# Kernel optimization log

Hardware: AMD Instinct MI355X
Metric: run time of the kernel (lower is better)

Reference implementation:

```python
import jax, jax.numpy as jnp
import numpy as np

QUERY_DIM = 1024
KEY_DIM = 768
NUM_HEADS = 16
HEAD_DIM = QUERY_DIM // NUM_HEADS


def _linear_params(key, in_dim, out_dim):
    kw, kb = jax.random.split(key)
    bound = 1.0 / np.sqrt(in_dim)
    W = jax.random.uniform(kw, (out_dim, in_dim), minval=-bound, maxval=bound, dtype=jnp.float32)
    b = jax.random.uniform(kb, (out_dim,), minval=-bound, maxval=bound, dtype=jnp.float32)
    return W, b


def setup_inputs() -> dict:
    key = jax.random.key(0)
    ks = jax.random.split(key, 7)
    B, Nq, Nk = 4, 1024, 2048
    query = jax.random.normal(ks[0], (B, Nq, QUERY_DIM), dtype=jnp.float32)
    k_in = jax.random.normal(ks[1], (B, Nk, KEY_DIM), dtype=jnp.float32)
    v_in = jax.random.normal(ks[2], (B, Nk, KEY_DIM), dtype=jnp.float32)
    Wq, bq = _linear_params(ks[3], QUERY_DIM, QUERY_DIM)
    Wk, bk = _linear_params(ks[4], KEY_DIM, QUERY_DIM)
    Wv, bv = _linear_params(ks[5], KEY_DIM, QUERY_DIM)
    Wo, bo = _linear_params(ks[6], QUERY_DIM, QUERY_DIM)
    return {
        "query": query, "key": k_in, "value": v_in,
        "Wq": Wq, "bq": bq, "Wk": Wk, "bk": bk,
        "Wv": Wv, "bv": bv, "Wo": Wo, "bo": bo,
    }


def reference(query, key, value, Wq, bq, Wk, bk, Wv, bv, Wo, bo):
    B, Nq, _ = query.shape
    Nk = key.shape[1]
    H, D = NUM_HEADS, HEAD_DIM
    scale = 1.0 / np.sqrt(D)
    # Projections (torch Linear: x @ W.T + b), then split heads -> (B, H, N, D)
    Q = (query @ Wq.T + bq).reshape(B, Nq, H, D).transpose(0, 2, 1, 3)
    K = (key @ Wk.T + bk).reshape(B, Nk, H, D).transpose(0, 2, 1, 3)
    V = (value @ Wv.T + bv).reshape(B, Nk, H, D).transpose(0, 2, 1, 3)
    # Explicit score matrix (B, H, Nq, Nk), softmax over keys
    attn = jnp.einsum('bhqd,bhkd->bhqk', Q, K) * scale
    attn = jax.nn.softmax(attn, axis=-1)
    out = jnp.einsum('bhqk,bhkd->bhqd', attn, V)
    out = out.transpose(0, 2, 1, 3).reshape(B, Nq, H * D)
    return out @ Wo.T + bo
```

## Files before the change

kernel.cpp:

```cpp
#include <hip/hip_runtime.h>
#include <stdint.h>


typedef __attribute__((ext_vector_type(4))) float f32x4;
typedef __attribute__((ext_vector_type(8))) _Float16 half8;
typedef __attribute__((ext_vector_type(4))) _Float16 half4;
typedef __attribute__((ext_vector_type(4))) short short4v;
typedef __attribute__((ext_vector_type(8))) short short8;
typedef unsigned short u16;

__device__ __forceinline__ u16 f2h(float f){
  _Float16 h = (_Float16)f;
  return __builtin_bit_cast(unsigned short, h);
}

__device__ __forceinline__ void gload16(const void* g, void* lds){
  __builtin_amdgcn_global_load_lds((const __attribute__((address_space(1))) void*)g,
                                   (__attribute__((address_space(3))) void*)lds, 16, 0, 0);
}

struct Seg { const float* s; u16* d; int n4; };
struct Cvt7 { Seg seg[7]; };

__global__ __launch_bounds__(256) void cvt_f32_f16(Cvt7 a){
  Seg sg = a.seg[blockIdx.y];
  const long stride = (long)gridDim.x * 256;
  for (long i = (long)blockIdx.x*256 + threadIdx.x; i < sg.n4; i += stride){
    f32x4 v = *(const f32x4*)(sg.s + i*4);
    short4v h;
    h[0] = (short)f2h(v[0]); h[1] = (short)f2h(v[1]);
    h[2] = (short)f2h(v[2]); h[3] = (short)f2h(v[3]);
    *(short4v*)(sg.d + i*4) = h;
  }
}

template<int R, int THREADS>
__device__ __forceinline__ void stage_tile(const char* gbase, long gstride, char* lds, int tid){
  const int w = tid >> 6, lane = tid & 63;
  #pragma unroll
  for (int it = 0; it < R*8/THREADS; ++it){
    int c  = it*THREADS + w*64 + lane;
    int r  = c >> 3;
    int bs = (c & 7) << 4;
    int sb = bs ^ ((r & 7) << 4);
    gload16(gbase + (long)r*gstride + sb, lds + (it*THREADS + w*64)*16);
  }
}

__device__ __forceinline__ void gemm64_mainloop(const u16* A, const u16* Bt, int K,
                                                int row0, int col0, int tid,
                                                char* Alds, char* Blds, f32x4 acc[2][4]){
  const int lane = tid & 63, w = tid >> 6;
  const int g = lane >> 4, lm = lane & 15;
  const int wr = (w >> 1) * 32, wc = (w & 1) * 64;
  const char* Ag = (const char*)A  + ((long)row0 * K) * 2;
  const char* Bg = (const char*)Bt + ((long)col0 * K) * 2;
  for (int k0 = 0; k0 < K; k0 += 64){
    stage_tile<64, 256>(Ag + k0*2, (long)K*2, Alds, tid);
    stage_tile<128, 256>(Bg + k0*2, (long)K*2, Blds, tid);
    __syncthreads();
    #pragma unroll
    for (int kk = 0; kk < 2; ++kk){
      half8 af[2], bfr[4];
      #pragma unroll
      for (int mi = 0; mi < 2; ++mi){
        int r = wr + mi*16 + lm;
        af[mi] = *(const half8*)(Alds + r*128 + ((kk*64 + g*16) ^ ((r & 7) << 4)));
      }
      #pragma unroll
      for (int ni = 0; ni < 4; ++ni){
        int r = wc + ni*16 + lm;
        bfr[ni] = *(const half8*)(Blds + r*128 + ((kk*64 + g*16) ^ ((r & 7) << 4)));
      }
      #pragma unroll
      for (int mi = 0; mi < 2; ++mi)
        #pragma unroll
        for (int ni = 0; ni < 4; ++ni)
          acc[mi][ni] = __builtin_amdgcn_mfma_f32_16x16x32_f16(af[mi], bfr[ni], acc[mi][ni], 0, 0, 0);
    }
    __syncthreads();
  }
}

__global__ __launch_bounds__(256, 4)
void qkv_proj(const u16* __restrict__ qH, const u16* __restrict__ kH, const u16* __restrict__ vH,
              const u16* __restrict__ WqH, const u16* __restrict__ WkH, const u16* __restrict__ WvH,
              const float* __restrict__ bq, const float* __restrict__ bk, const float* __restrict__ bv,
              u16* __restrict__ Qw, u16* __restrict__ Kw, u16* __restrict__ Vtw)
{
  __shared__ __align__(128) char Alds[8192];
  __shared__ __align__(128) char Blds[16384];
  const int tid = threadIdx.x, lane = tid & 63, w = tid >> 6;
  const int g = lane >> 4, lm = lane & 15;

  int bid = blockIdx.x;
  const u16 *A, *Bt; const float* bias; u16* out16;
  int K, logS, local; float scale = 1.0f;
  int which;
  if (bid < 512)       { which = 0; local = bid;        A = qH; Bt = WqH; bias = bq; out16 = Qw;  K = 1024; logS = 10; scale = 0.125f; }
  else if (bid < 1536) { which = 1; local = bid - 512;  A = kH; Bt = WkH; bias = bk; out16 = Kw;  K = 768;  logS = 11; }
  else                 { which = 2; local = bid - 1536; A = vH; Bt = WvH; bias = bv; out16 = Vtw; K = 768;  logS = 11; }
  const int rb = local >> 3, cb = local & 7;
  const int row0 = rb * 64, col0 = cb * 128;

  f32x4 acc[2][4];
  #pragma unroll
  for (int i = 0; i < 2; ++i)
    #pragma unroll
    for (int j = 0; j < 4; ++j) acc[i][j] = {0.f, 0.f, 0.f, 0.f};

  gemm64_mainloop(A, Bt, K, row0, col0, tid, Alds, Blds, acc);

  const int wr = (w >> 1) * 32, wc = (w & 1) * 64;
  if (which != 2){
    #pragma unroll
    for (int mi = 0; mi < 2; ++mi)
      #pragma unroll
      for (int ni = 0; ni < 4; ++ni){
        int n = col0 + wc + ni*16 + lm;
        float bvv = bias[n];
        int h_ = n >> 6, d_ = n & 63;
        #pragma unroll
        for (int r = 0; r < 4; ++r){
          int m = row0 + wr + mi*16 + g*4 + r;
          int b_ = m >> logS, s_ = m & ((1 << logS) - 1);
          long dst = (((long)(b_*16 + h_) << logS) + s_) * 64 + d_;
          out16[dst] = f2h((acc[mi][ni][r] + bvv) * scale);
        }
      }
  } else {
    #pragma unroll
    for (int mi = 0; mi < 2; ++mi)
      #pragma unroll
      for (int ni = 0; ni < 4; ++ni){
        int np = wc + ni*16 + lm;
        float bvv = bias[col0 + np];
        short4v h4;
        #pragma unroll
        for (int r = 0; r < 4; ++r) h4[r] = (short)f2h(acc[mi][ni][r] + bvv);
        int mb = (wr + mi*16 + g*4) * 2;
        *(short4v*)(Blds + np*128 + (mb ^ ((np & 7) << 4))) = h4;
      }
    __syncthreads();
    const int b_ = row0 >> 11;
    #pragma unroll
    for (int pass = 0; pass < 4; ++pass){
      int idx = pass*256 + tid, row = idx >> 3, c = idx & 7;
      short8 v = *(const short8*)(Blds + row*128 + ((c*16) ^ ((row & 7) << 4)));
      int ng = col0 + row, h_ = ng >> 6, d_ = ng & 63;
      long dst = ((long)(b_*16 + h_)*64 + d_)*2048 + (row0 & 2047) + c*8;
      *(short8*)(out16 + dst) = v;
    }
  }
}

__global__ __launch_bounds__(512, 4)
void attn_fused(const u16* __restrict__ Qw, const u16* __restrict__ Kw,
                const u16* __restrict__ Vtw, u16* __restrict__ AO)
{
  __shared__ __align__(128) char Klds[8192];
  __shared__ __align__(128) char Vlds[8192];
  const int tid = threadIdx.x, lane = tid & 63, w = tid >> 6;
  const int g = lane >> 4, lm = lane & 15;
  const int p = blockIdx.x;
  const int slot = p >> 3;
  const int bh = (p & 7) + ((slot & 7) << 3);
  const int qt = slot >> 3;
  const long qbase = (long)bh * 1024 * 64;
  const long kbase = (long)bh * 2048 * 64;
  const long vbase = (long)bh * 64 * 2048;

  const int q0 = qt*128 + w*16;
  half8 aQ[2];
  #pragma unroll
  for (int kk = 0; kk < 2; ++kk)
    aQ[kk] = *(const half8*)((const char*)Qw + (qbase + (long)(q0 + lm)*64 + kk*32 + g*8)*2);

  float mrun = -3e38f, lrun = 0.f;
  f32x4 O[4];
  #pragma unroll
  for (int di = 0; di < 4; ++di) O[di] = {0.f, 0.f, 0.f, 0.f};

  for (int kt = 0; kt < 2048; kt += 64){
    stage_tile<64, 512>((const char*)Kw  + (kbase + (long)kt*64)*2, 128,  Klds, tid);
    stage_tile<64, 512>((const char*)Vtw + (vbase + kt)*2,          4096, Vlds, tid);
    __syncthreads();

    half8 kf[4][2];
    #pragma unroll
    for (int t = 0; t < 4; ++t)
      #pragma unroll
      for (int kk = 0; kk < 2; ++kk){
        int r = t*16 + lm;
        kf[t][kk] = *(const half8*)(Klds + r*128 + ((kk*64 + g*16) ^ ((r & 7) << 4)));
      }

    f32x4 sc[4];
    #pragma unroll
    for (int t = 0; t < 4; ++t){
      f32x4 z = {0.f, 0.f, 0.f, 0.f};
      z = __builtin_amdgcn_mfma_f32_16x16x32_f16(kf[t][0], aQ[0], z, 0, 0, 0);
      z = __builtin_amdgcn_mfma_f32_16x16x32_f16(kf[t][1], aQ[1], z, 0, 0, 0);
      sc[t] = z;
    }
    float pm = sc[0][0];
    #pragma unroll
    for (int t = 0; t < 4; ++t)
      #pragma unroll
      for (int r = 0; r < 4; ++r) pm = fmaxf(pm, sc[t][r]);
    pm = fmaxf(pm, __shfl_xor(pm, 16));
    pm = fmaxf(pm, __shfl_xor(pm, 32));
    float mnew = fmaxf(mrun, pm);
    float fac  = __expf(mrun - mnew);
    float ls = 0.f;
    #pragma unroll
    for (int t = 0; t < 4; ++t)
      #pragma unroll
      for (int r = 0; r < 4; ++r){ float pv = __expf(sc[t][r] - mnew); sc[t][r] = pv; ls += pv; }
    ls += __shfl_xor(ls, 16);
    ls += __shfl_xor(ls, 32);
    lrun = lrun*fac + ls;
    mrun = mnew;
    float frow[4];
    #pragma unroll
    for (int r = 0; r < 4; ++r) frow[r] = __shfl(fac, (lane & 48) | (g*4 + r));
    #pragma unroll
    for (int di = 0; di < 4; ++di){
      O[di][0] *= frow[0]; O[di][1] *= frow[1];
      O[di][2] *= frow[2]; O[di][3] *= frow[3];
    }
    half8 pa[2];
    #pragma unroll
    for (int kh = 0; kh < 2; ++kh)
      #pragma unroll
      for (int i = 0; i < 8; ++i){
        int t = kh*2 + (i >> 2), r = i & 3;
        pa[kh][i] = (_Float16)sc[t][r];
      }
    #pragma unroll
    for (int di = 0; di < 4; ++di){
      int d = di*16 + lm;
      int swz = (d & 7) << 4;
      #pragma unroll
      for (int kh = 0; kh < 2; ++kh){
        half4 lo = *(const half4*)(Vlds + d*128 + ((kh*64 + g*8)      ^ swz));
        half4 hi = *(const half4*)(Vlds + d*128 + ((kh*64 + g*8 + 32) ^ swz));
        half8 vf = { lo[0], lo[1], lo[2], lo[3], hi[0], hi[1], hi[2], hi[3] };
        O[di] = __builtin_amdgcn_mfma_f32_16x16x32_f16(pa[kh], vf, O[di], 0, 0, 0);
      }
    }
    __syncthreads();
  }

  const int b = bh >> 4, h = bh & 15;
  float inv = 1.f / lrun;
  float irow[4];
  #pragma unroll
  for (int r = 0; r < 4; ++r) irow[r] = __shfl(inv, (lane & 48) | (g*4 + r));
  #pragma unroll
  for (int di = 0; di < 4; ++di)
    #pragma unroll
    for (int r = 0; r < 4; ++r){
      long q = q0 + g*4 + r;
      AO[((long)b*1024 + q)*1024 + h*64 + di*16 + lm] = f2h(O[di][r] * irow[r]);
    }
}

__global__ __launch_bounds__(256, 4)
void gemm_o(const u16* __restrict__ A, const u16* __restrict__ Bt,
            const float* __restrict__ bias, float* __restrict__ outF)
{
  __shared__ __align__(128) char Alds[8192];
  __shared__ __align__(128) char Blds[16384];
  const int tid = threadIdx.x, lane = tid & 63, w = tid >> 6;
  const int g = lane >> 4, lm = lane & 15;
  const int rb = blockIdx.x >> 3, cb = blockIdx.x & 7;
  const int row0 = rb * 64, col0 = cb * 128;

  f32x4 acc[2][4];
  #pragma unroll
  for (int i = 0; i < 2; ++i)
    #pragma unroll
    for (int j = 0; j < 4; ++j) acc[i][j] = {0.f, 0.f, 0.f, 0.f};

  gemm64_mainloop(A, Bt, 1024, row0, col0, tid, Alds, Blds, acc);

  const int wr = (w >> 1) * 32, wc = (w & 1) * 64;
  #pragma unroll
  for (int mi = 0; mi < 2; ++mi)
    #pragma unroll
    for (int ni = 0; ni < 4; ++ni){
      int n = col0 + wc + ni*16 + lm;
      float bvv = bias[n];
      #pragma unroll
      for (int r = 0; r < 4; ++r){
        int m = row0 + wr + mi*16 + g*4 + r;
        outF[(long)m * 1024 + n] = acc[mi][ni][r] + bvv;
      }
    }
}

extern "C" void kernel_launch(void* const* d_in, const int* in_sizes, int n_in,
                              void* d_out, int out_size, void* d_ws, size_t ws_size,
                              hipStream_t stream)
{
  const float* query = (const float*)d_in[0];
  const float* key   = (const float*)d_in[1];
  const float* value = (const float*)d_in[2];
  const float* Wq = (const float*)d_in[3];
  const float* bq = (const float*)d_in[4];
  const float* Wk = (const float*)d_in[5];
  const float* bk = (const float*)d_in[6];
  const float* Wv = (const float*)d_in[7];
  const float* bv = (const float*)d_in[8];
  const float* Wo = (const float*)d_in[9];
  const float* bo = (const float*)d_in[10];
  float* out = (float*)d_out;

  char* p = (char*)d_ws;
  auto alloc = [&](long bytes){ char* r = p; p += bytes; return r; };
  u16* qH  = (u16*)alloc( 8l<<20);
  u16* kH  = (u16*)alloc(12l<<20);
  u16* vH  = (u16*)alloc(12l<<20);
  u16* WqH = (u16*)alloc( 2l<<20);
  u16* WkH = (u16*)alloc( 2l<<20);
  u16* WvH = (u16*)alloc( 2l<<20);
  u16* WoH = (u16*)alloc( 2l<<20);
  u16* Qw  = (u16*)alloc( 8l<<20);
  u16* Kw  = (u16*)alloc(16l<<20);
  u16* Vtw = (u16*)alloc(16l<<20);
  u16* AO  = (u16*)alloc( 8l<<20);

  Cvt7 ca;
  ca.seg[0] = { query, qH,  4096*1024/4 };
  ca.seg[1] = { key,   kH,  8192*768/4  };
  ca.seg[2] = { value, vH,  8192*768/4  };
  ca.seg[3] = { Wq,    WqH, 1024*1024/4 };
  ca.seg[4] = { Wk,    WkH, 1024*768/4  };
  ca.seg[5] = { Wv,    WvH, 1024*768/4  };
  ca.seg[6] = { Wo,    WoH, 1024*1024/4 };
  cvt_f32_f16<<<dim3(512, 7), 256, 0, stream>>>(ca);

  qkv_proj<<<dim3(2560), dim3(256), 0, stream>>>(qH, kH, vH, WqH, WkH, WvH,
                                                 bq, bk, bv, Qw, Kw, Vtw);
  attn_fused<<<dim3(512), dim3(512), 0, stream>>>(Qw, Kw, Vtw, AO);
  gemm_o<<<dim3(512), dim3(256), 0, stream>>>(AO, WoH, bo, out);
}
```

Measured before the change: 267.6 us.

## Double-buffer LDS tiles, remap blocks for XCDs, add lazy softmax rescale

Both GEMM mainloops and the attention loop now use double-buffered LDS. The next K tile is issued with global_load_lds before the current tile is computed, and partial vmcnt waits with raw barriers replace the __syncthreads pairs. Block IDs in the QKV and output GEMMs are remapped so neighbouring tiles land on the same XCD. Attention skips the running-max rescale unless the new max exceeds the old by more than 8, and packs P to half with cvt_pkrtz. The doubled LDS lowers the GEMM occupancy hint from 4 to 3 blocks, and the lazy rescale allows somewhat larger intermediate values.

```diff
diff --git a/kernel.cpp b/kernel.cpp
--- a/kernel.cpp
+++ b/kernel.cpp
@@ -5,6 +5,7 @@
 typedef __attribute__((ext_vector_type(4))) float f32x4;
 typedef __attribute__((ext_vector_type(8))) _Float16 half8;
 typedef __attribute__((ext_vector_type(4))) _Float16 half4;
+typedef __attribute__((ext_vector_type(2))) _Float16 half2v;
 typedef __attribute__((ext_vector_type(4))) short short4v;
 typedef __attribute__((ext_vector_type(8))) short short8;
 typedef unsigned short u16;
@@ -47,30 +48,42 @@
   }
 }
 
-__device__ __forceinline__ void gemm64_mainloop(const u16* A, const u16* Bt, int K,
-                                                int row0, int col0, int tid,
-                                                char* Alds, char* Blds, f32x4 acc[2][4]){
+__device__ __forceinline__ void gemm64_pipe(const u16* A, const u16* Bt, int K,
+                                            int row0, int col0, int tid,
+                                            char* lds, f32x4 acc[2][4]){
   const int lane = tid & 63, w = tid >> 6;
   const int g = lane >> 4, lm = lane & 15;
   const int wr = (w >> 1) * 32, wc = (w & 1) * 64;
   const char* Ag = (const char*)A  + ((long)row0 * K) * 2;
   const char* Bg = (const char*)Bt + ((long)col0 * K) * 2;
+
+  stage_tile<64, 256>(Ag, (long)K*2, lds, tid);
+  stage_tile<128, 256>(Bg, (long)K*2, lds + 8192, tid);
+
   for (int k0 = 0; k0 < K; k0 += 64){
-    stage_tile<64, 256>(Ag + k0*2, (long)K*2, Alds, tid);
-    stage_tile<128, 256>(Bg + k0*2, (long)K*2, Blds, tid);
-    __syncthreads();
+    char* cur = lds + ((k0 >> 6) & 1) * 24576;
+    if (k0 + 64 < K){
+      char* nxt = lds + ((((k0 >> 6) & 1) ^ 1)) * 24576;
+      stage_tile<64, 256>(Ag + (long)(k0+64)*2, (long)K*2, nxt, tid);
+      stage_tile<128, 256>(Bg + (long)(k0+64)*2, (long)K*2, nxt + 8192, tid);
+      asm volatile("s_waitcnt vmcnt(6)" ::: "memory");
+    } else {
+      asm volatile("s_waitcnt vmcnt(0)" ::: "memory");
+    }
+    __builtin_amdgcn_s_barrier();
+    char* Al = cur, *Bl = cur + 8192;
     #pragma unroll
     for (int kk = 0; kk < 2; ++kk){
       half8 af[2], bfr[4];
       #pragma unroll
       for (int mi = 0; mi < 2; ++mi){
         int r = wr + mi*16 + lm;
-        af[mi] = *(const half8*)(Alds + r*128 + ((kk*64 + g*16) ^ ((r & 7) << 4)));
+        af[mi] = *(const half8*)(Al + r*128 + ((kk*64 + g*16) ^ ((r & 7) << 4)));
       }
       #pragma unroll
       for (int ni = 0; ni < 4; ++ni){
         int r = wc + ni*16 + lm;
-        bfr[ni] = *(const half8*)(Blds + r*128 + ((kk*64 + g*16) ^ ((r & 7) << 4)));
+        bfr[ni] = *(const half8*)(Bl + r*128 + ((kk*64 + g*16) ^ ((r & 7) << 4)));
       }
       #pragma unroll
       for (int mi = 0; mi < 2; ++mi)
@@ -78,22 +91,21 @@
         for (int ni = 0; ni < 4; ++ni)
           acc[mi][ni] = __builtin_amdgcn_mfma_f32_16x16x32_f16(af[mi], bfr[ni], acc[mi][ni], 0, 0, 0);
     }
-    __syncthreads();
-  }
-}
-
-__global__ __launch_bounds__(256, 4)
+    __builtin_amdgcn_s_barrier();
+  }
+}
+
+__global__ __launch_bounds__(256, 3)
 void qkv_proj(const u16* __restrict__ qH, const u16* __restrict__ kH, const u16* __restrict__ vH,
               const u16* __restrict__ WqH, const u16* __restrict__ WkH, const u16* __restrict__ WvH,
               const float* __restrict__ bq, const float* __restrict__ bk, const float* __restrict__ bv,
               u16* __restrict__ Qw, u16* __restrict__ Kw, u16* __restrict__ Vtw)
 {
-  __shared__ __align__(128) char Alds[8192];
-  __shared__ __align__(128) char Blds[16384];
+  __shared__ __align__(128) char lds[49152];
   const int tid = threadIdx.x, lane = tid & 63, w = tid >> 6;
   const int g = lane >> 4, lm = lane & 15;
 
-  int bid = blockIdx.x;
+  int bid = (blockIdx.x & 7) * 320 + (blockIdx.x >> 3);
   const u16 *A, *Bt; const float* bias; u16* out16;
   int K, logS, local; float scale = 1.0f;
   int which;
@@ -109,7 +121,7 @@
     #pragma unroll
     for (int j = 0; j < 4; ++j) acc[i][j] = {0.f, 0.f, 0.f, 0.f};
 
-  gemm64_mainloop(A, Bt, K, row0, col0, tid, Alds, Blds, acc);
+  gemm64_pipe(A, Bt, K, row0, col0, tid, lds, acc);
 
   const int wr = (w >> 1) * 32, wc = (w & 1) * 64;
   if (which != 2){
@@ -139,14 +151,14 @@
         #pragma unroll
         for (int r = 0; r < 4; ++r) h4[r] = (short)f2h(acc[mi][ni][r] + bvv);
         int mb = (wr + mi*16 + g*4) * 2;
-        *(short4v*)(Blds + np*128 + (mb ^ ((np & 7) << 4))) = h4;
+        *(short4v*)(lds + np*128 + (mb ^ ((np & 7) << 4))) = h4;
       }
     __syncthreads();
     const int b_ = row0 >> 11;
     #pragma unroll
     for (int pass = 0; pass < 4; ++pass){
       int idx = pass*256 + tid, row = idx >> 3, c = idx & 7;
-      short8 v = *(const short8*)(Blds + row*128 + ((c*16) ^ ((row & 7) << 4)));
+      short8 v = *(const short8*)(lds + row*128 + ((c*16) ^ ((row & 7) << 4)));
       int ng = col0 + row, h_ = ng >> 6, d_ = ng & 63;
       long dst = ((long)(b_*16 + h_)*64 + d_)*2048 + (row0 & 2047) + c*8;
       *(short8*)(out16 + dst) = v;
@@ -158,8 +170,7 @@
 void attn_fused(const u16* __restrict__ Qw, const u16* __restrict__ Kw,
                 const u16* __restrict__ Vtw, u16* __restrict__ AO)
 {
-  __shared__ __align__(128) char Klds[8192];
-  __shared__ __align__(128) char Vlds[8192];
+  __shared__ __align__(128) char lds[32768];
   const int tid = threadIdx.x, lane = tid & 63, w = tid >> 6;
   const int g = lane >> 4, lm = lane & 15;
   const int p = blockIdx.x;
@@ -181,10 +192,21 @@
   #pragma unroll
   for (int di = 0; di < 4; ++di) O[di] = {0.f, 0.f, 0.f, 0.f};
 
+  stage_tile<64, 512>((const char*)Kw  + kbase*2, 128,  lds, tid);
+  stage_tile<64, 512>((const char*)Vtw + vbase*2, 4096, lds + 8192, tid);
+
   for (int kt = 0; kt < 2048; kt += 64){
-    stage_tile<64, 512>((const char*)Kw  + (kbase + (long)kt*64)*2, 128,  Klds, tid);
-    stage_tile<64, 512>((const char*)Vtw + (vbase + kt)*2,          4096, Vlds, tid);
-    __syncthreads();
+    char* cur = lds + ((kt >> 6) & 1) * 16384;
+    if (kt + 64 < 2048){
+      char* nxt = lds + ((((kt >> 6) & 1) ^ 1)) * 16384;
+      stage_tile<64, 512>((const char*)Kw  + (kbase + (long)(kt+64)*64)*2, 128,  nxt, tid);
+      stage_tile<64, 512>((const char*)Vtw + (vbase + kt+64)*2,            4096, nxt + 8192, tid);
+      asm volatile("s_waitcnt vmcnt(2)" ::: "memory");
+    } else {
+      asm volatile("s_waitcnt vmcnt(0)" ::: "memory");
+    }
+    __builtin_amdgcn_s_barrier();
+    char* Klds = cur, *Vlds = cur + 8192;
 
     half8 kf[4][2];
     #pragma unroll
@@ -210,32 +232,39 @@
       for (int r = 0; r < 4; ++r) pm = fmaxf(pm, sc[t][r]);
     pm = fmaxf(pm, __shfl_xor(pm, 16));
     pm = fmaxf(pm, __shfl_xor(pm, 32));
-    float mnew = fmaxf(mrun, pm);
-    float fac  = __expf(mrun - mnew);
+    if (!__all(pm <= mrun + 8.0f)){
+      float mnew = fmaxf(mrun, pm);
+      float fac  = __expf(mrun - mnew);
+      lrun *= fac;
+      float frow[4];
+      #pragma unroll
+      for (int r = 0; r < 4; ++r) frow[r] = __shfl(fac, (lane & 48) | (g*4 + r));
+      #pragma unroll
+      for (int di = 0; di < 4; ++di){
+        O[di][0] *= frow[0]; O[di][1] *= frow[1];
+        O[di][2] *= frow[2]; O[di][3] *= frow[3];
+      }
+      mrun = mnew;
+    }
     float ls = 0.f;
     #pragma unroll
     for (int t = 0; t < 4; ++t)
       #pragma unroll
-      for (int r = 0; r < 4; ++r){ float pv = __expf(sc[t][r] - mnew); sc[t][r] = pv; ls += pv; }
+      for (int r = 0; r < 4; ++r){ float pv = __expf(sc[t][r] - mrun); sc[t][r] = pv; ls += pv; }
     ls += __shfl_xor(ls, 16);
     ls += __shfl_xor(ls, 32);
-    lrun = lrun*fac + ls;
-    mrun = mnew;
-    float frow[4];
-    #pragma unroll
-    for (int r = 0; r < 4; ++r) frow[r] = __shfl(fac, (lane & 48) | (g*4 + r));
-    #pragma unroll
-    for (int di = 0; di < 4; ++di){
-      O[di][0] *= frow[0]; O[di][1] *= frow[1];
-      O[di][2] *= frow[2]; O[di][3] *= frow[3];
-    }
+    lrun += ls;
+
     half8 pa[2];
     #pragma unroll
     for (int kh = 0; kh < 2; ++kh)
       #pragma unroll
-      for (int i = 0; i < 8; ++i){
-        int t = kh*2 + (i >> 2), r = i & 3;
-        pa[kh][i] = (_Float16)sc[t][r];
+      for (int j = 0; j < 2; ++j){
+        int t = kh*2 + j;
+        half2v p01 = __builtin_bit_cast(half2v, __builtin_amdgcn_cvt_pkrtz(sc[t][0], sc[t][1]));
+        half2v p23 = __builtin_bit_cast(half2v, __builtin_amdgcn_cvt_pkrtz(sc[t][2], sc[t][3]));
+        pa[kh][j*4+0] = p01[0]; pa[kh][j*4+1] = p01[1];
+        pa[kh][j*4+2] = p23[0]; pa[kh][j*4+3] = p23[1];
       }
     #pragma unroll
     for (int di = 0; di < 4; ++di){
@@ -249,7 +278,7 @@
         O[di] = __builtin_amdgcn_mfma_f32_16x16x32_f16(pa[kh], vf, O[di], 0, 0, 0);
       }
     }
-    __syncthreads();
+    __builtin_amdgcn_s_barrier();
   }
 
   const int b = bh >> 4, h = bh & 15;
@@ -266,15 +295,15 @@
     }
 }
 
-__global__ __launch_bounds__(256, 4)
+__global__ __launch_bounds__(256, 3)
 void gemm_o(const u16* __restrict__ A, const u16* __restrict__ Bt,
             const float* __restrict__ bias, float* __restrict__ outF)
 {
-  __shared__ __align__(128) char Alds[8192];
-  __shared__ __align__(128) char Blds[16384];
+  __shared__ __align__(128) char lds[49152];
   const int tid = threadIdx.x, lane = tid & 63, w = tid >> 6;
   const int g = lane >> 4, lm = lane & 15;
-  const int rb = blockIdx.x >> 3, cb = blockIdx.x & 7;
+  int bid = (blockIdx.x & 7) * 64 + (blockIdx.x >> 3);
+  const int rb = bid >> 3, cb = bid & 7;
   const int row0 = rb * 64, col0 = cb * 128;
 
   f32x4 acc[2][4];
@@ -283,7 +312,7 @@
     #pragma unroll
     for (int j = 0; j < 4; ++j) acc[i][j] = {0.f, 0.f, 0.f, 0.f};
 
-  gemm64_mainloop(A, Bt, 1024, row0, col0, tid, Alds, Blds, acc);
+  gemm64_pipe(A, Bt, 1024, row0, col0, tid, lds, acc);
 
   const int wr = (w >> 1) * 32, wc = (w & 1) * 64;
   #pragma unroll
```

After: 256.7 us. 4.1% less time.
